# Kernel optimization log

Hardware: AMD Instinct MI355X
Metric: run time of the kernel (lower is better)

The kernel has to match this reference:

```python
import jax, jax.numpy as jnp
import numpy as np

B, I, H, N, E, SEQ = 16, 128, 32, 2048, 32768, 100


def setup_inputs() -> dict:
    key = jax.random.key(0)
    ks = jax.random.split(key, 8)
    s = lambda fan: 1.0 / np.sqrt(fan)
    return {
        "x": jax.random.normal(ks[0], (B, I), jnp.float32),
        "src": jax.random.randint(ks[1], (E,), 0, N, jnp.int32),
        "dst": jax.random.randint(ks[2], (E,), 0, N, jnp.int32),
        "Wr": jax.random.normal(ks[3], (I, H), jnp.float32) * s(I),
        "br": jnp.zeros((H,), jnp.float32),
        "Wz": jax.random.normal(ks[4], (I, H), jnp.float32) * s(I),
        "bz": jnp.zeros((H,), jnp.float32),
        "Wh": jax.random.normal(ks[5], (I, H), jnp.float32) * s(I),
        "bh": jnp.zeros((H,), jnp.float32),
        "Wg": jax.random.normal(ks[6], (H, H), jnp.float32) * s(H),
        "bg": jnp.zeros((H,), jnp.float32),
    }


def reference(x, src, dst, Wr, br, Wz, bz, Wh, bh, Wg, bg):
    # DGL GraphConv norm='both': edge weight 1/sqrt(deg_out[src]*deg_in[dst])
    ones = jnp.ones((E,), jnp.float32)
    deg_out = jnp.clip(jax.ops.segment_sum(ones, src, num_segments=N), 1.0)
    deg_in = jnp.clip(jax.ops.segment_sum(ones, dst, num_segments=N), 1.0)
    enorm = jax.lax.rsqrt(deg_out[src] * deg_in[dst])  # [E]

    # Input gates are constant over time (x is a single context vector)
    xr = (x @ Wr + br)[:, None, :]  # [B,1,H]
    xz = (x @ Wz + bz)[:, None, :]
    xh = (x @ Wh + bh)[:, None, :]

    def step(h, _):
        # message passing: gather src, normalize, scatter-add to dst
        m = h[:, src, :] * enorm[None, :, None]            # [B,E,H]
        agg = jnp.zeros_like(h).at[:, dst, :].add(m)       # [B,N,H]
        h_conv = agg @ Wg + bg                             # [B,N,H]
        r = jax.nn.sigmoid(xr + h_conv)
        z = jax.nn.sigmoid(xz + h_conv)
        h_tilde = jnp.tanh(xh + r * h_conv)
        h_new = (1.0 - z) * h + z * h_tilde
        return h_new, h_new

    h0 = jnp.zeros((B, N, H), jnp.float32)
    _, outs = jax.lax.scan(step, h0, None, length=SEQ)     # [SEQ,B,N,H]
    return jnp.transpose(outs, (1, 0, 2, 3)).reshape(B, -1)
```

## Files before the change

kernel.cpp:

```cpp
#include <hip/hip_runtime.h>
#include <math.h>

#define BATCH 16
#define IN 128
#define HD 32
#define NN 2048
#define NE 32768
#define SEQ 100
#define TPB 512
#define NBLK 512
#define GSZ 32
#define NGRP (NBLK / GSZ)
#define NXCD 8
#define MAXJ 64
#define ECAP 1536


__global__ void count_deg(const int* __restrict__ src, const int* __restrict__ dst,
                          int* deg_out, int* deg_in) {
    int e = blockIdx.x * blockDim.x + threadIdx.x;
    if (e < NE) {
        atomicAdd(&deg_out[src[e]], 1);
        atomicAdd(&deg_in[dst[e]], 1);
    }
}

__global__ void scan_rowptr(const int* __restrict__ deg_in, int* __restrict__ row_ptr) {
    __shared__ int partial[256];
    int t = threadIdx.x;
    int base = t * 8;
    int vals[8];
    int s = 0;
    for (int j = 0; j < 8; j++) { vals[j] = deg_in[base + j]; s += vals[j]; }
    partial[t] = s;
    __syncthreads();
    if (t == 0) {
        int acc = 0;
        for (int i = 0; i < 256; i++) { int v = partial[i]; partial[i] = acc; acc += v; }
        row_ptr[NN] = acc;
    }
    __syncthreads();
    int acc = partial[t];
    for (int j = 0; j < 8; j++) { row_ptr[base + j] = acc; acc += vals[j]; }
}

__global__ void scatter_edges(const int* __restrict__ src, const int* __restrict__ dst,
                              const int* __restrict__ deg_out, const int* __restrict__ deg_in,
                              const int* __restrict__ row_ptr, int* __restrict__ cursor,
                              int* __restrict__ col_idx, float* __restrict__ wgt) {
    int e = blockIdx.x * blockDim.x + threadIdx.x;
    if (e < NE) {
        int s = src[e], d = dst[e];
        int pos = row_ptr[d] + atomicAdd(&cursor[d], 1);
        col_idx[pos] = s * HD;
        float doo = (float)max(deg_out[s], 1);
        float dii = (float)max(deg_in[d], 1);
        wgt[pos] = rsqrtf(doo * dii);
    }
}

__global__ void xgates(const float* __restrict__ x,
                       const float* __restrict__ Wr, const float* __restrict__ br,
                       const float* __restrict__ Wz, const float* __restrict__ bz,
                       const float* __restrict__ Wh, const float* __restrict__ bh,
                       float* __restrict__ xr, float* __restrict__ xz, float* __restrict__ xh) {
    int t = blockIdx.x * blockDim.x + threadIdx.x;
    if (t < BATCH * HD) {
        int b = t / HD, hh = t % HD;
        float ar = br[hh], az = bz[hh], ah = bh[hh];
        const float* xb = x + b * IN;
        for (int i = 0; i < IN; i++) {
            float xv = xb[i];
            ar += xv * Wr[i * HD + hh];
            az += xv * Wz[i * HD + hh];
            ah += xv * Wh[i * HD + hh];
        }
        xr[t] = ar; xz[t] = az; xh[t] = ah;
    }
}


__device__ __forceinline__ void global_barrier(unsigned* __restrict__ lvl1,
                                               unsigned* __restrict__ root,
                                               unsigned step) {
    __syncthreads();
    if (threadIdx.x == 0) {
        const int gid = blockIdx.x / GSZ;
        __builtin_amdgcn_fence(__ATOMIC_RELEASE, "agent");
        __hip_atomic_fetch_add(&lvl1[gid * 32], 1u, __ATOMIC_RELAXED,
                               __HIP_MEMORY_SCOPE_AGENT);
        if ((blockIdx.x % GSZ) == 0) {
            while (__hip_atomic_load(&lvl1[gid * 32], __ATOMIC_RELAXED,
                                     __HIP_MEMORY_SCOPE_AGENT) < GSZ * step)
                __builtin_amdgcn_s_sleep(2);
            __hip_atomic_fetch_add(root, 1u, __ATOMIC_RELAXED,
                                   __HIP_MEMORY_SCOPE_AGENT);
        }
        while (__hip_atomic_load(root, __ATOMIC_RELAXED,
                                 __HIP_MEMORY_SCOPE_AGENT) < NGRP * step)
            __builtin_amdgcn_s_sleep(2);
        __builtin_amdgcn_fence(__ATOMIC_ACQUIRE, "agent");
    }
    __syncthreads();
}

__device__ __forceinline__ void xcd_barrier(unsigned* __restrict__ xcnt,
                                            unsigned* __restrict__ xgo,
                                            int xid, int slot, int cnt, unsigned s) {
    __syncthreads();
    if (threadIdx.x == 0) {
        __hip_atomic_fetch_add(&xcnt[(xid * 8 + (slot & 7)) * 32], 1u,
                               __ATOMIC_RELAXED, __HIP_MEMORY_SCOPE_AGENT);
        if (slot == 0) {
            for (;;) {
                unsigned sum = 0;
#pragma unroll
                for (int i = 0; i < 8; i++)
                    sum += __hip_atomic_load(&xcnt[(xid * 8 + i) * 32],
                                             __ATOMIC_RELAXED, __HIP_MEMORY_SCOPE_AGENT);
                if (sum >= (unsigned)cnt * s) break;
                __builtin_amdgcn_s_sleep(1);
            }
            __hip_atomic_store(&xgo[xid * 32], s, __ATOMIC_RELAXED,
                               __HIP_MEMORY_SCOPE_AGENT);
        } else {
            while (__hip_atomic_load(&xgo[xid * 32], __ATOMIC_RELAXED,
                                     __HIP_MEMORY_SCOPE_AGENT) < s)
                __builtin_amdgcn_s_sleep(1);
        }
    }
    __syncthreads();
    asm volatile("buffer_inv sc0\n\ts_waitcnt vmcnt(0)" ::: "memory");
}


__device__ __forceinline__ float fast_sigmoid(float x) {
    return __builtin_amdgcn_rcpf(1.f + __expf(-x));
}

__global__ void __launch_bounds__(TPB) gru_persistent(
    float* __restrict__ hA, float* __restrict__ hB,
    const int* __restrict__ row_ptr, const int* __restrict__ col_idx,
    const float* __restrict__ wgt,
    const float* __restrict__ Wg, const float* __restrict__ bg,
    const float* __restrict__ xr, const float* __restrict__ xz,
    const float* __restrict__ xh,
    float* __restrict__ out,
    unsigned* __restrict__ glvl1, unsigned* __restrict__ groot,
    unsigned* __restrict__ xreg, unsigned* __restrict__ xcnt,
    unsigned* __restrict__ xgo)
{
    __shared__ float aggL[TPB];
    __shared__ int jn[MAXJ], jrs[MAXJ], jraw[MAXJ], jplen[MAXJ], jofs[MAXJ];
    __shared__ __align__(16) int2 eLDS[ECAP];
    __shared__ int shr_slot, shr_cnt, shr_mode, shr_use;

    const int tid = threadIdx.x;
    const int lane = tid & 63;
    const int wid = tid >> 6;
    const int half = lane >> 5;
    const int l = lane & 31;

    int xraw;
    asm volatile("s_getreg_b32 %0, hwreg(HW_REG_XCC_ID)" : "=s"(xraw));
    int xid = xraw & 7;

    if (tid == 0)
        shr_slot = (int)__hip_atomic_fetch_add(&xreg[xid * 32], 1u, __ATOMIC_RELAXED,
                                               __HIP_MEMORY_SCOPE_AGENT);
    __syncthreads();
    int slot = shr_slot;

    global_barrier(glvl1, groot, 1u);

    if (tid == 0) {
        int sum = 0, mode = 1, mycnt = 0;
        for (int xx = 0; xx < NXCD; xx++) {
            int c = (int)__hip_atomic_load(&xreg[xx * 32], __ATOMIC_RELAXED,
                                           __HIP_MEMORY_SCOPE_AGENT);
            sum += c;
            if (c < 32) mode = 0;
            if (xx == xid) mycnt = c;
        }
        if (sum != NBLK) mode = 0;
        shr_mode = mode;
        shr_cnt = mycnt;
    }
    __syncthreads();
    const int xmode = shr_mode;
    int cnt = shr_cnt;
    if (!xmode) { xid = blockIdx.x & 7; slot = blockIdx.x >> 3; cnt = NBLK / NXCD; }
    const int wtot = cnt * 8;

    if (tid < MAXJ) {
        int k = tid >> 3, w = tid & 7;
        int n = slot * 8 + w + k * wtot;
        if (n < NN) {
            int rs = row_ptr[n], re = row_ptr[n + 1];
            jn[tid] = n; jrs[tid] = rs; jraw[tid] = re - rs;
            jplen[tid] = (re - rs + 7) & ~7;
        } else {
            jn[tid] = -1; jrs[tid] = 0; jraw[tid] = 0; jplen[tid] = 0;
        }
    }
    __syncthreads();
    if (tid == 0) {
        int o = 0;
        for (int j = 0; j < MAXJ; j++) { jofs[j] = o; o += jplen[j]; }
        shr_use = (o <= ECAP);
    }
    __syncthreads();
    const bool use_lds = (shr_use != 0);

    if (use_lds) {
        for (int k = 0; k < 8; k++) {
            int j = k * 8 + wid;
            if (jn[j] < 0) break;
            int rs = jrs[j], raw = jraw[j], pl = jplen[j], of = jofs[j];
            for (int i = lane; i < pl; i += 64) {
                int2 v;
                if (i < raw) { v.x = col_idx[rs + i] << 2; v.y = __float_as_int(wgt[rs + i]); }
                else         { v.x = 0; v.y = 0; }
                eLDS[of + i] = v;
            }
        }
    }
    __syncthreads();

    const int bb = 2 * xid + half;
    const float xrv = xr[bb * HD + l];
    const float xzv = xz[bb * HD + l];
    const float xhv = xh[bb * HD + l];
    const float bgv = bg[l];
    float wgreg[HD];
#pragma unroll
    for (int k = 0; k < HD; k++) wgreg[k] = Wg[k * HD + l];

    const int hoffb = (bb * (NN * HD) + l) * 4;
    float* outp = out + (size_t)bb * SEQ * (NN * HD) + l;

    const char* hprev = (const char*)hA;
    char* hnext = (char*)hB;

    for (int t = 0; t < SEQ; t++) {
        for (int k = 0; k < 8; k++) {
            const int j = k * 8 + wid;
            const int n = jn[j];
            if (n < 0) break;

            float agg = 0.f;
            if (use_lds) {
                const int4* ep = (const int4*)&eLDS[jofs[j]];
                const int pl = jplen[j];
                int e = 0;
                for (; e + 16 <= pl; e += 16) {
                    int4 p0 = ep[0], p1 = ep[1], p2 = ep[2], p3 = ep[3];
                    int4 p4 = ep[4], p5 = ep[5], p6 = ep[6], p7 = ep[7];
                    ep += 8;
                    float v0 = *(const float*)(hprev + (hoffb + p0.x));
                    float v1 = *(const float*)(hprev + (hoffb + p0.z));
                    float v2 = *(const float*)(hprev + (hoffb + p1.x));
                    float v3 = *(const float*)(hprev + (hoffb + p1.z));
                    float v4 = *(const float*)(hprev + (hoffb + p2.x));
                    float v5 = *(const float*)(hprev + (hoffb + p2.z));
                    float v6 = *(const float*)(hprev + (hoffb + p3.x));
                    float v7 = *(const float*)(hprev + (hoffb + p3.z));
                    float v8 = *(const float*)(hprev + (hoffb + p4.x));
                    float v9 = *(const float*)(hprev + (hoffb + p4.z));
                    float va = *(const float*)(hprev + (hoffb + p5.x));
                    float vb = *(const float*)(hprev + (hoffb + p5.z));
                    float vc = *(const float*)(hprev + (hoffb + p6.x));
                    float vd = *(const float*)(hprev + (hoffb + p6.z));
                    float ve = *(const float*)(hprev + (hoffb + p7.x));
                    float vf = *(const float*)(hprev + (hoffb + p7.z));
                    agg = fmaf(__int_as_float(p0.y), v0, agg);
                    agg = fmaf(__int_as_float(p0.w), v1, agg);
                    agg = fmaf(__int_as_float(p1.y), v2, agg);
                    agg = fmaf(__int_as_float(p1.w), v3, agg);
                    agg = fmaf(__int_as_float(p2.y), v4, agg);
                    agg = fmaf(__int_as_float(p2.w), v5, agg);
                    agg = fmaf(__int_as_float(p3.y), v6, agg);
                    agg = fmaf(__int_as_float(p3.w), v7, agg);
                    agg = fmaf(__int_as_float(p4.y), v8, agg);
                    agg = fmaf(__int_as_float(p4.w), v9, agg);
                    agg = fmaf(__int_as_float(p5.y), va, agg);
                    agg = fmaf(__int_as_float(p5.w), vb, agg);
                    agg = fmaf(__int_as_float(p6.y), vc, agg);
                    agg = fmaf(__int_as_float(p6.w), vd, agg);
                    agg = fmaf(__int_as_float(p7.y), ve, agg);
                    agg = fmaf(__int_as_float(p7.w), vf, agg);
                }
                if (e < pl) {
                    int4 p0 = ep[0], p1 = ep[1], p2 = ep[2], p3 = ep[3];
                    float v0 = *(const float*)(hprev + (hoffb + p0.x));
                    float v1 = *(const float*)(hprev + (hoffb + p0.z));
                    float v2 = *(const float*)(hprev + (hoffb + p1.x));
                    float v3 = *(const float*)(hprev + (hoffb + p1.z));
                    float v4 = *(const float*)(hprev + (hoffb + p2.x));
                    float v5 = *(const float*)(hprev + (hoffb + p2.z));
                    float v6 = *(const float*)(hprev + (hoffb + p3.x));
                    float v7 = *(const float*)(hprev + (hoffb + p3.z));
                    agg = fmaf(__int_as_float(p0.y), v0, agg);
                    agg = fmaf(__int_as_float(p0.w), v1, agg);
                    agg = fmaf(__int_as_float(p1.y), v2, agg);
                    agg = fmaf(__int_as_float(p1.w), v3, agg);
                    agg = fmaf(__int_as_float(p2.y), v4, agg);
                    agg = fmaf(__int_as_float(p2.w), v5, agg);
                    agg = fmaf(__int_as_float(p3.y), v6, agg);
                    agg = fmaf(__int_as_float(p3.w), v7, agg);
                }
            } else {
                const int rs = jrs[j], re = rs + jraw[j];
                for (int e = rs; e < re; e++) {
                    int cb = col_idx[e] << 2;
                    agg = fmaf(wgt[e], *(const float*)(hprev + (hoffb + cb)), agg);
                }
            }

            aggL[tid] = agg;
            const float4* arow = (const float4*)&aggL[(tid & ~63) + (half << 5)];
            float conv = bgv;
#pragma unroll
            for (int kq = 0; kq < 8; kq++) {
                float4 a4 = arow[kq];
                conv = fmaf(a4.x, wgreg[4 * kq + 0], conv);
                conv = fmaf(a4.y, wgreg[4 * kq + 1], conv);
                conv = fmaf(a4.z, wgreg[4 * kq + 2], conv);
                conv = fmaf(a4.w, wgreg[4 * kq + 3], conv);
            }

            const float r = fast_sigmoid(xrv + conv);
            const float z = fast_sigmoid(xzv + conv);
            const float e2 = __expf(2.f * (xhv + r * conv));
            const float ht = 1.f - 2.f * __builtin_amdgcn_rcpf(e2 + 1.f);
            const int nb = hoffb + (n << 7);
            const float hp = *(const float*)(hprev + nb);
            const float hn = fmaf(z, ht - hp, hp);

            *(float*)(hnext + nb) = hn;
            __builtin_nontemporal_store(hn, outp + (n << 5));
        }
        if (t != SEQ - 1) {
            if (xmode)
                xcd_barrier(xcnt, xgo, xid, slot, cnt, (unsigned)(t + 1));
            else
                global_barrier(glvl1, groot, (unsigned)(t + 2));
        }
        char* tmp = (char*)hprev; hprev = hnext; hnext = tmp;
        outp += NN * HD;
    }
}


extern "C" void kernel_launch(void* const* d_in, const int* in_sizes, int n_in,
                              void* d_out, int out_size, void* d_ws, size_t ws_size,
                              hipStream_t stream) {
    const float* x   = (const float*)d_in[0];
    const int*   src = (const int*)d_in[1];
    const int*   dst = (const int*)d_in[2];
    const float* Wr  = (const float*)d_in[3];
    const float* br  = (const float*)d_in[4];
    const float* Wz  = (const float*)d_in[5];
    const float* bz  = (const float*)d_in[6];
    const float* Wh  = (const float*)d_in[7];
    const float* bh  = (const float*)d_in[8];
    const float* Wg  = (const float*)d_in[9];
    const float* bg  = (const float*)d_in[10];
    float* out = (float*)d_out;

    char* ws = (char*)d_ws;
    float* h0 = (float*)ws;            ws += (size_t)BATCH * NN * HD * 4;
    float* h1 = (float*)ws;            ws += (size_t)BATCH * NN * HD * 4;
    float* xr = (float*)ws;            ws += BATCH * HD * 4;
    float* xz = (float*)ws;            ws += BATCH * HD * 4;
    float* xh = (float*)ws;            ws += BATCH * HD * 4;
    int* deg_out = (int*)ws;           ws += NN * 4;
    int* deg_in  = (int*)ws;           ws += NN * 4;
    int* cursor  = (int*)ws;           ws += NN * 4;
    int* row_ptr = (int*)ws;           ws += (NN + 1) * 4;
    int* col_idx = (int*)ws;           ws += NE * 4;
    float* wgt   = (float*)ws;         ws += NE * 4;
    unsigned* glvl1 = (unsigned*)ws;   ws += NGRP * 32 * 4;
    unsigned* groot = (unsigned*)ws;   ws += 32 * 4;
    unsigned* xreg  = (unsigned*)ws;   ws += NXCD * 32 * 4;
    unsigned* xcnt  = (unsigned*)ws;   ws += NXCD * 8 * 32 * 4;
    unsigned* xgo   = (unsigned*)ws;   ws += NXCD * 32 * 4;

    hipMemsetAsync(h0, 0, (size_t)BATCH * NN * HD * 4, stream);
    hipMemsetAsync(deg_out, 0, 3 * NN * 4, stream);
    hipMemsetAsync(glvl1, 0,
                   (NGRP * 32 + 32 + NXCD * 32 + NXCD * 8 * 32 + NXCD * 32) * 4, stream);

    count_deg<<<NE / 256, 256, 0, stream>>>(src, dst, deg_out, deg_in);
    scan_rowptr<<<1, 256, 0, stream>>>(deg_in, row_ptr);
    scatter_edges<<<NE / 256, 256, 0, stream>>>(src, dst, deg_out, deg_in, row_ptr,
                                                cursor, col_idx, wgt);
    xgates<<<2, 256, 0, stream>>>(x, Wr, br, Wz, bz, Wh, bh, xr, xz, xh);

    gru_persistent<<<dim3(NBLK), dim3(TPB), 0, stream>>>(
        h0, h1, row_ptr, col_idx, wgt, Wg, bg, xr, xz, xh, out,
        glvl1, groot, xreg, xcnt, xgo);
}
```

Baseline: 740.5 us.

## Use output buffer as hidden state and specialize zero-state first step

The hidden-state ping-pong buffers are removed, and each step reads the previous hidden state straight from the previous timestep's slice of the output tensor. Each step then does a single normal store instead of one workspace store plus one nontemporal output store, and the memset of h0 goes away. Step 0 is computed in closed form from the zero initial state, which skips the gather for that step. Edge padding is reduced from multiples of 8 to multiples of 2, with a 2-wide tail loop, so fewer zero-weight gathers run. In exchange, output writes are now cached loads and stores over a large buffer, which may raise cache pressure compared with streaming nontemporal stores.

```diff
diff --git a/kernel.cpp b/kernel.cpp
--- a/kernel.cpp
+++ b/kernel.cpp
@@ -14,6 +14,7 @@
 #define NXCD 8
 #define MAXJ 64
 #define ECAP 1536
+#define STEPB (NN * HD * 4)
 
 
 __global__ void count_deg(const int* __restrict__ src, const int* __restrict__ dst,
@@ -139,7 +140,6 @@
 }
 
 __global__ void __launch_bounds__(TPB) gru_persistent(
-    float* __restrict__ hA, float* __restrict__ hB,
     const int* __restrict__ row_ptr, const int* __restrict__ col_idx,
     const float* __restrict__ wgt,
     const float* __restrict__ Wg, const float* __restrict__ bg,
@@ -198,7 +198,7 @@
         if (n < NN) {
             int rs = row_ptr[n], re = row_ptr[n + 1];
             jn[tid] = n; jrs[tid] = rs; jraw[tid] = re - rs;
-            jplen[tid] = (re - rs + 7) & ~7;
+            jplen[tid] = (re - rs + 1) & ~1;
         } else {
             jn[tid] = -1; jrs[tid] = 0; jraw[tid] = 0; jplen[tid] = 0;
         }
@@ -236,13 +236,27 @@
 #pragma unroll
     for (int k = 0; k < HD; k++) wgreg[k] = Wg[k * HD + l];
 
-    const int hoffb = (bb * (NN * HD) + l) * 4;
-    float* outp = out + (size_t)bb * SEQ * (NN * HD) + l;
-
-    const char* hprev = (const char*)hA;
-    char* hnext = (char*)hB;
-
-    for (int t = 0; t < SEQ; t++) {
+    char* const outc = (char*)out;
+    unsigned ocur = (unsigned)(bb * SEQ) * STEPB + (unsigned)(l * 4);
+
+    {
+        const float conv = bgv;
+        const float z = fast_sigmoid(xzv + conv);
+        const float e2 = __expf(2.f * (xhv + fast_sigmoid(xrv + conv) * conv));
+        const float ht = 1.f - 2.f * __builtin_amdgcn_rcpf(e2 + 1.f);
+        const float hn = z * ht;
+        for (int k = 0; k < 8; k++) {
+            const int n = jn[k * 8 + wid];
+            if (n < 0) break;
+            *(float*)(outc + (ocur + ((unsigned)n << 7))) = hn;
+        }
+    }
+    if (xmode) xcd_barrier(xcnt, xgo, xid, slot, cnt, 1u);
+    else       global_barrier(glvl1, groot, 2u);
+    ocur += STEPB;
+
+    for (int t = 1; t < SEQ; t++) {
+        const char* opc = outc + (ocur - STEPB);
         for (int k = 0; k < 8; k++) {
             const int j = k * 8 + wid;
             const int n = jn[j];
@@ -257,22 +271,22 @@
                     int4 p0 = ep[0], p1 = ep[1], p2 = ep[2], p3 = ep[3];
                     int4 p4 = ep[4], p5 = ep[5], p6 = ep[6], p7 = ep[7];
                     ep += 8;
-                    float v0 = *(const float*)(hprev + (hoffb + p0.x));
-                    float v1 = *(const float*)(hprev + (hoffb + p0.z));
-                    float v2 = *(const float*)(hprev + (hoffb + p1.x));
-                    float v3 = *(const float*)(hprev + (hoffb + p1.z));
-                    float v4 = *(const float*)(hprev + (hoffb + p2.x));
-                    float v5 = *(const float*)(hprev + (hoffb + p2.z));
-                    float v6 = *(const float*)(hprev + (hoffb + p3.x));
-                    float v7 = *(const float*)(hprev + (hoffb + p3.z));
-                    float v8 = *(const float*)(hprev + (hoffb + p4.x));
-                    float v9 = *(const float*)(hprev + (hoffb + p4.z));
-                    float va = *(const float*)(hprev + (hoffb + p5.x));
-                    float vb = *(const float*)(hprev + (hoffb + p5.z));
-                    float vc = *(const float*)(hprev + (hoffb + p6.x));
-                    float vd = *(const float*)(hprev + (hoffb + p6.z));
-                    float ve = *(const float*)(hprev + (hoffb + p7.x));
-                    float vf = *(const float*)(hprev + (hoffb + p7.z));
+                    float v0 = *(const float*)(opc + (unsigned)p0.x);
+                    float v1 = *(const float*)(opc + (unsigned)p0.z);
+                    float v2 = *(const float*)(opc + (unsigned)p1.x);
+                    float v3 = *(const float*)(opc + (unsigned)p1.z);
+                    float v4 = *(const float*)(opc + (unsigned)p2.x);
+                    float v5 = *(const float*)(opc + (unsigned)p2.z);
+                    float v6 = *(const float*)(opc + (unsigned)p3.x);
+                    float v7 = *(const float*)(opc + (unsigned)p3.z);
+                    float v8 = *(const float*)(opc + (unsigned)p4.x);
+                    float v9 = *(const float*)(opc + (unsigned)p4.z);
+                    float va = *(const float*)(opc + (unsigned)p5.x);
+                    float vb = *(const float*)(opc + (unsigned)p5.z);
+                    float vc = *(const float*)(opc + (unsigned)p6.x);
+                    float vd = *(const float*)(opc + (unsigned)p6.z);
+                    float ve = *(const float*)(opc + (unsigned)p7.x);
+                    float vf = *(const float*)(opc + (unsigned)p7.z);
                     agg = fmaf(__int_as_float(p0.y), v0, agg);
                     agg = fmaf(__int_as_float(p0.w), v1, agg);
                     agg = fmaf(__int_as_float(p1.y), v2, agg);
@@ -290,30 +304,18 @@
                     agg = fmaf(__int_as_float(p7.y), ve, agg);
                     agg = fmaf(__int_as_float(p7.w), vf, agg);
                 }
-                if (e < pl) {
-                    int4 p0 = ep[0], p1 = ep[1], p2 = ep[2], p3 = ep[3];
-                    float v0 = *(const float*)(hprev + (hoffb + p0.x));
-                    float v1 = *(const float*)(hprev + (hoffb + p0.z));
-                    float v2 = *(const float*)(hprev + (hoffb + p1.x));
-                    float v3 = *(const float*)(hprev + (hoffb + p1.z));
-                    float v4 = *(const float*)(hprev + (hoffb + p2.x));
-                    float v5 = *(const float*)(hprev + (hoffb + p2.z));
-                    float v6 = *(const float*)(hprev + (hoffb + p3.x));
-                    float v7 = *(const float*)(hprev + (hoffb + p3.z));
+                for (; e < pl; e += 2) {
+                    int4 p0 = *ep++;
+                    float v0 = *(const float*)(opc + (unsigned)p0.x);
+                    float v1 = *(const float*)(opc + (unsigned)p0.z);
                     agg = fmaf(__int_as_float(p0.y), v0, agg);
                     agg = fmaf(__int_as_float(p0.w), v1, agg);
-                    agg = fmaf(__int_as_float(p1.y), v2, agg);
-                    agg = fmaf(__int_as_float(p1.w), v3, agg);
-                    agg = fmaf(__int_as_float(p2.y), v4, agg);
-                    agg = fmaf(__int_as_float(p2.w), v5, agg);
-                    agg = fmaf(__int_as_float(p3.y), v6, agg);
-                    agg = fmaf(__int_as_float(p3.w), v7, agg);
                 }
             } else {
                 const int rs = jrs[j], re = rs + jraw[j];
                 for (int e = rs; e < re; e++) {
-                    int cb = col_idx[e] << 2;
-                    agg = fmaf(wgt[e], *(const float*)(hprev + (hoffb + cb)), agg);
+                    unsigned cb = (unsigned)col_idx[e] << 2;
+                    agg = fmaf(wgt[e], *(const float*)(opc + cb), agg);
                 }
             }
 
@@ -333,21 +335,17 @@
             const float z = fast_sigmoid(xzv + conv);
             const float e2 = __expf(2.f * (xhv + r * conv));
             const float ht = 1.f - 2.f * __builtin_amdgcn_rcpf(e2 + 1.f);
-            const int nb = hoffb + (n << 7);
-            const float hp = *(const float*)(hprev + nb);
+            const unsigned nb = (unsigned)n << 7;
+            const float hp = *(const float*)(opc + nb);
             const float hn = fmaf(z, ht - hp, hp);
 
-            *(float*)(hnext + nb) = hn;
-            __builtin_nontemporal_store(hn, outp + (n << 5));
+            *(float*)(outc + (ocur + nb)) = hn;
         }
         if (t != SEQ - 1) {
-            if (xmode)
-                xcd_barrier(xcnt, xgo, xid, slot, cnt, (unsigned)(t + 1));
-            else
-                global_barrier(glvl1, groot, (unsigned)(t + 2));
-        }
-        char* tmp = (char*)hprev; hprev = hnext; hnext = tmp;
-        outp += NN * HD;
+            if (xmode) xcd_barrier(xcnt, xgo, xid, slot, cnt, (unsigned)(t + 1));
+            else       global_barrier(glvl1, groot, (unsigned)(t + 2));
+        }
+        ocur += STEPB;
     }
 }
 
@@ -369,8 +367,6 @@
     float* out = (float*)d_out;
 
     char* ws = (char*)d_ws;
-    float* h0 = (float*)ws;            ws += (size_t)BATCH * NN * HD * 4;
-    float* h1 = (float*)ws;            ws += (size_t)BATCH * NN * HD * 4;
     float* xr = (float*)ws;            ws += BATCH * HD * 4;
     float* xz = (float*)ws;            ws += BATCH * HD * 4;
     float* xh = (float*)ws;            ws += BATCH * HD * 4;
@@ -386,7 +382,6 @@
     unsigned* xcnt  = (unsigned*)ws;   ws += NXCD * 8 * 32 * 4;
     unsigned* xgo   = (unsigned*)ws;   ws += NXCD * 32 * 4;
 
-    hipMemsetAsync(h0, 0, (size_t)BATCH * NN * HD * 4, stream);
     hipMemsetAsync(deg_out, 0, 3 * NN * 4, stream);
     hipMemsetAsync(glvl1, 0,
                    (NGRP * 32 + 32 + NXCD * 32 + NXCD * 8 * 32 + NXCD * 32) * 4, stream);
@@ -398,6 +393,6 @@
     xgates<<<2, 256, 0, stream>>>(x, Wr, br, Wz, bz, Wh, bh, xr, xz, xh);
 
     gru_persistent<<<dim3(NBLK), dim3(TPB), 0, stream>>>(
-        h0, h1, row_ptr, col_idx, wgt, Wg, bg, xr, xz, xh, out,
+        row_ptr, col_idx, wgt, Wg, bg, xr, xz, xh, out,
         glvl1, groot, xreg, xcnt, xgo);
 }
```

Result: slower. 961.0 us (+29.8%).

## Specialize first GRU step for zero state and pad edge lists to pairs

Applied to the files above, without the earlier changes.

Because h starts at zero, the first time step's aggregation is zero, so that step is computed in closed form from the biases and written directly. This skips one full gather pass and the memset of the initial hidden buffer. Edge lists in LDS are now padded to multiples of 2 instead of 8, with a tail loop that handles two edges per iteration, which cuts wasted padded gathers. The tail loop adds a little loop overhead, and the barrier epoch numbering must stay consistent with the new first step.

```diff
diff --git a/kernel.cpp b/kernel.cpp
--- a/kernel.cpp
+++ b/kernel.cpp
@@ -198,7 +198,7 @@
         if (n < NN) {
             int rs = row_ptr[n], re = row_ptr[n + 1];
             jn[tid] = n; jrs[tid] = rs; jraw[tid] = re - rs;
-            jplen[tid] = (re - rs + 7) & ~7;
+            jplen[tid] = (re - rs + 1) & ~1;
         } else {
             jn[tid] = -1; jrs[tid] = 0; jraw[tid] = 0; jplen[tid] = 0;
         }
@@ -242,7 +242,26 @@
     const char* hprev = (const char*)hA;
     char* hnext = (char*)hB;
 
-    for (int t = 0; t < SEQ; t++) {
+    {
+        const float conv = bgv;
+        const float r = fast_sigmoid(xrv + conv);
+        const float z = fast_sigmoid(xzv + conv);
+        const float e2 = __expf(2.f * (xhv + r * conv));
+        const float ht = 1.f - 2.f * __builtin_amdgcn_rcpf(e2 + 1.f);
+        const float hn = z * ht;
+        for (int k = 0; k < 8; k++) {
+            const int n = jn[k * 8 + wid];
+            if (n < 0) break;
+            *(float*)(hnext + (hoffb + (n << 7))) = hn;
+            __builtin_nontemporal_store(hn, outp + (n << 5));
+        }
+    }
+    if (xmode) xcd_barrier(xcnt, xgo, xid, slot, cnt, 1u);
+    else       global_barrier(glvl1, groot, 2u);
+    { char* tmp = (char*)hprev; hprev = hnext; hnext = tmp; }
+    outp += NN * HD;
+
+    for (int t = 1; t < SEQ; t++) {
         for (int k = 0; k < 8; k++) {
             const int j = k * 8 + wid;
             const int n = jn[j];
@@ -290,24 +309,12 @@
                     agg = fmaf(__int_as_float(p7.y), ve, agg);
                     agg = fmaf(__int_as_float(p7.w), vf, agg);
                 }
-                if (e < pl) {
-                    int4 p0 = ep[0], p1 = ep[1], p2 = ep[2], p3 = ep[3];
+                for (; e < pl; e += 2) {
+                    int4 p0 = *ep++;
                     float v0 = *(const float*)(hprev + (hoffb + p0.x));
                     float v1 = *(const float*)(hprev + (hoffb + p0.z));
-                    float v2 = *(const float*)(hprev + (hoffb + p1.x));
-                    float v3 = *(const float*)(hprev + (hoffb + p1.z));
-                    float v4 = *(const float*)(hprev + (hoffb + p2.x));
-                    float v5 = *(const float*)(hprev + (hoffb + p2.z));
-                    float v6 = *(const float*)(hprev + (hoffb + p3.x));
-                    float v7 = *(const float*)(hprev + (hoffb + p3.z));
                     agg = fmaf(__int_as_float(p0.y), v0, agg);
                     agg = fmaf(__int_as_float(p0.w), v1, agg);
-                    agg = fmaf(__int_as_float(p1.y), v2, agg);
-                    agg = fmaf(__int_as_float(p1.w), v3, agg);
-                    agg = fmaf(__int_as_float(p2.y), v4, agg);
-                    agg = fmaf(__int_as_float(p2.w), v5, agg);
-                    agg = fmaf(__int_as_float(p3.y), v6, agg);
-                    agg = fmaf(__int_as_float(p3.w), v7, agg);
                 }
             } else {
                 const int rs = jrs[j], re = rs + jraw[j];
@@ -341,10 +348,8 @@
             __builtin_nontemporal_store(hn, outp + (n << 5));
         }
         if (t != SEQ - 1) {
-            if (xmode)
-                xcd_barrier(xcnt, xgo, xid, slot, cnt, (unsigned)(t + 1));
-            else
-                global_barrier(glvl1, groot, (unsigned)(t + 2));
+            if (xmode) xcd_barrier(xcnt, xgo, xid, slot, cnt, (unsigned)(t + 1));
+            else       global_barrier(glvl1, groot, (unsigned)(t + 2));
         }
         char* tmp = (char*)hprev; hprev = hnext; hnext = tmp;
         outp += NN * HD;
@@ -386,7 +391,6 @@
     unsigned* xcnt  = (unsigned*)ws;   ws += NXCD * 8 * 32 * 4;
     unsigned* xgo   = (unsigned*)ws;   ws += NXCD * 32 * 4;
 
-    hipMemsetAsync(h0, 0, (size_t)BATCH * NN * HD * 4, stream);
     hipMemsetAsync(deg_out, 0, 3 * NN * 4, stream);
     hipMemsetAsync(glvl1, 0,
                    (NGRP * 32 + 32 + NXCD * 32 + NXCD * 8 * 32 + NXCD * 32) * 4, stream);
```

Measured after the change: 894.2 us. +20.8%, slower.
